# Kernel optimization log

Measured on AMD Instinct MI355X. Metric: run time of the kernel, lower is better.

## Reference

```python
import jax, jax.numpy as jnp
import numpy as np

D_MODEL = 768
D_HIDDEN = 2048
N_HEADS = 12
D_HEAD = 64
REG_COEFF = 1e-3
EPS = 1e-6
BATCH = 4
SEQ = 128


def setup_inputs() -> dict:
    key = jax.random.key(0)
    ks = jax.random.split(key, 4)
    # kaiming_uniform_ on (fan_in, fan_out)-shaped tensors: bound = sqrt(6 / fan_in_torch)
    # (values only need to be plausible; exact init dist is irrelevant for the kernel baseline)
    s_enc = 1.0 / np.sqrt(D_MODEL)
    s_dec = 1.0 / np.sqrt(D_HIDDEN)
    return {
        "x": jax.random.normal(ks[0], (BATCH, SEQ, D_MODEL), dtype=jnp.float32),
        "W_encQ": jax.random.normal(ks[1], (D_MODEL, D_HIDDEN), dtype=jnp.float32) * s_enc,
        "W_encK": jax.random.normal(ks[2], (D_MODEL, D_HIDDEN), dtype=jnp.float32) * s_enc,
        "b_encQ": jnp.zeros((D_HIDDEN,), dtype=jnp.float32),
        "b_encK": jnp.zeros((D_HIDDEN,), dtype=jnp.float32),
        "W_dec": jax.random.normal(ks[3], (D_HIDDEN, N_HEADS), dtype=jnp.float32) * s_dec,
        "b_dec": jnp.zeros((N_HEADS,), dtype=jnp.float32),
    }


def reference(x, W_encQ, W_encK, b_encQ, b_encK, W_dec, b_dec):
    # queries/keys: (batch, posn, d_hidden)
    queries = jax.nn.relu(jnp.einsum("bsd,dh->bsh", x, W_encQ) + b_encQ)
    keys = jax.nn.relu(jnp.einsum("bsd,dh->bsh", x, W_encK) + b_encK)
    # acts: (batch, posn_q, posn_k, d_hidden) -- the huge multi-use intermediate
    acts = queries[:, :, None, :] * keys[:, None, :, :]
    reg_loss = REG_COEFF * jnp.sum(jnp.sqrt(jnp.abs(acts) + EPS))
    feature_fires = (acts > 0).astype(jnp.int32)
    # decode to per-head scores: (batch, posn_q, posn_k, n_heads)
    score = jnp.einsum("bqkh,hn->bqkn", acts, W_dec) / np.sqrt(D_HEAD) + b_dec
    score = jnp.transpose(score, (0, 3, 1, 2))  # (batch, n_heads, posn_q, posn_k)
    return score, reg_loss, feature_fires
```

## Files before the change

### kernel.cpp

```cpp
#include <hip/hip_runtime.h>
#include <hip/hip_bf16.h>

#define D_MODEL 768
#define D_HIDDEN 2048
#define NHEADS 12
#define BATCH 4
#define SEQ 128
#define MROWS (BATCH*SEQ)
#define SCORE_ELEMS (BATCH*NHEADS*SEQ*SEQ)
#define REG_OFF SCORE_ELEMS
#define FIRES_OFF (SCORE_ELEMS + 1)
#define NROWS_T 65536
#define FIRES_WAVES 2048
#define FIRES_BLOCKS 512
#define SCORE_BLOCKS (BATCH*NHEADS*16)
#define REG_BLOCKS 512
#define TRIGCAP 64

typedef __attribute__((ext_vector_type(8))) short bf16x8;
typedef __attribute__((ext_vector_type(4))) float f32x4;

static __device__ __forceinline__ unsigned short f2bf(float f) {
    union { float f; unsigned u; } v; v.f = f;
    unsigned u = v.u;
    return (unsigned short)((u + 0x7FFFu + ((u >> 16) & 1u)) >> 16);
}

static __device__ __forceinline__ void split_bf16(float v, short& hi, short& lo) {
    unsigned short h = f2bf(v);
    float hf = __uint_as_float((unsigned)h << 16);
    float lf = v - hf;
    hi = (short)h;
    lo = (short)f2bf(lf);
}

static __device__ __forceinline__ float fsqrt_fast(float x) {
    return __builtin_amdgcn_sqrtf(x);
}

__global__ __launch_bounds__(256) void enc_kernel(
    const float* __restrict__ x,
    const float* __restrict__ WQ, const float* __restrict__ WK,
    const float* __restrict__ bQ, const float* __restrict__ bK,
    float* __restrict__ qbuf, float* __restrict__ kbuf,
    float* __restrict__ out)
{
    __shared__ unsigned tcnt;
    __shared__ unsigned tlist[TRIGCAP];
    __shared__ double   redd[4];

    const int bufid = blockIdx.z;
    const float* W    = bufid ? WK : WQ;
    const float* bias = bufid ? bK : bQ;
    float* outbuf     = bufid ? kbuf : qbuf;

    const int t  = threadIdx.x;
    if (t == 0) tcnt = 0u;
    if (blockIdx.x == 0 && blockIdx.y == 0 && blockIdx.z == 0 && t == 0)
        out[REG_OFF] = 0.f;
    __syncthreads();

    const int w  = t >> 6;
    const int l  = t & 63;
    const int mt = blockIdx.y * 64 + (w >> 1) * 32;
    const int nt = blockIdx.x * 64 + (w & 1) * 32;
    const int lr = l & 15;
    const int hg = (l >> 4) * 8;

    f32x4 acc[2][2];
    #pragma unroll
    for (int i = 0; i < 2; ++i)
        #pragma unroll
        for (int j = 0; j < 2; ++j) { f32x4 z = {0.f, 0.f, 0.f, 0.f}; acc[i][j] = z; }

    for (int kk = 0; kk < D_MODEL; kk += 32) {
        const int h0 = kk + hg;
        bf16x8 ah[2], al[2], bh[2], bl[2];
        #pragma unroll
        for (int fi = 0; fi < 2; ++fi) {
            const float* xp = x + (size_t)(mt + fi * 16 + lr) * D_MODEL + h0;
            const float4 v1 = *reinterpret_cast<const float4*>(xp);
            const float4 v2 = *reinterpret_cast<const float4*>(xp + 4);
            const float vv[8] = {v1.x, v1.y, v1.z, v1.w, v2.x, v2.y, v2.z, v2.w};
            #pragma unroll
            for (int i = 0; i < 8; ++i) {
                short h_, lo_;
                split_bf16(vv[i], h_, lo_);
                ah[fi][i] = h_; al[fi][i] = lo_;
            }
        }
        #pragma unroll
        for (int fj = 0; fj < 2; ++fj) {
            const int col = nt + fj * 16 + lr;
            #pragma unroll
            for (int i = 0; i < 8; ++i) {
                short h_, lo_;
                split_bf16(W[(size_t)(h0 + i) * D_HIDDEN + col], h_, lo_);
                bh[fj][i] = h_; bl[fj][i] = lo_;
            }
        }
        #pragma unroll
        for (int fi = 0; fi < 2; ++fi)
            #pragma unroll
            for (int fj = 0; fj < 2; ++fj) {
                acc[fi][fj] = __builtin_amdgcn_mfma_f32_16x16x32_bf16(
                    ah[fi], bh[fj], acc[fi][fj], 0, 0, 0);
                acc[fi][fj] = __builtin_amdgcn_mfma_f32_16x16x32_bf16(
                    ah[fi], bl[fj], acc[fi][fj], 0, 0, 0);
                acc[fi][fj] = __builtin_amdgcn_mfma_f32_16x16x32_bf16(
                    al[fi], bh[fj], acc[fi][fj], 0, 0, 0);
            }
    }

    #pragma unroll
    for (int fi = 0; fi < 2; ++fi)
        #pragma unroll
        for (int fj = 0; fj < 2; ++fj)
            #pragma unroll
            for (int j = 0; j < 4; ++j) {
                const int row = mt + fi * 16 + (l >> 4) * 4 + j;
                const int col = nt + fj * 16 + lr;
                float pre = acc[fi][fj][j] + bias[col];
                if (fabsf(pre) < 3e-4f) {
                    unsigned idx = atomicAdd(&tcnt, 1u);
                    if (idx < TRIGCAP) {
                        tlist[idx] = ((unsigned)row << 11) | (unsigned)col;
                    } else {
                        const float* xr = x + (size_t)row * D_MODEL;
                        const float* wc = W + col;
                        double s = (double)bias[col];
                        for (int dd = 0; dd < D_MODEL; ++dd)
                            s += (double)xr[dd] * (double)wc[(size_t)dd * D_HIDDEN];
                        pre = (float)s;
                    }
                }
                outbuf[(size_t)row * D_HIDDEN + col] = fmaxf(pre, 0.f);
            }

    __syncthreads();
    const unsigned n = min(tcnt, (unsigned)TRIGCAP);
    for (unsigned i = 0; i < n; ++i) {
        const unsigned e = tlist[i];
        const int hh = (int)(e & 2047u);
        const int mm = (int)(e >> 11);
        double s = 0.0;
        #pragma unroll
        for (int k = 0; k < 3; ++k) {
            const int dd = t + k * 256;
            s += (double)x[(size_t)mm * D_MODEL + dd]
               * (double)W[(size_t)dd * D_HIDDEN + hh];
        }
        #pragma unroll
        for (int off = 32; off > 0; off >>= 1) s += __shfl_down(s, off);
        if (l == 0) redd[w] = s;
        __syncthreads();
        if (t == 0) {
            double tot = redd[0] + redd[1] + redd[2] + redd[3] + (double)bias[hh];
            outbuf[(size_t)mm * D_HIDDEN + hh] = fmaxf((float)tot, 0.f);
        }
        __syncthreads();
    }
}

__global__ __launch_bounds__(128) void mask_kernel(
    const float* __restrict__ qbuf, const float* __restrict__ kbuf,
    unsigned* __restrict__ qmask, unsigned* __restrict__ kmask)
{
    const int r = blockIdx.x;
    const int t = threadIdx.x;
    const int l = t & 63;
    const float* src = (t < 64) ? qbuf : kbuf;
    unsigned* dst    = (t < 64) ? qmask : kmask;
    unsigned m = 0;
    #pragma unroll
    for (int j = 0; j < 8; ++j)
        #pragma unroll
        for (int e = 0; e < 4; ++e) {
            const float v = src[(size_t)r * D_HIDDEN + 256 * j + 4 * l + e];
            m |= (v > 0.f ? 1u : 0u) << (4 * j + e);
        }
    dst[r * 64 + l] = m;
}

__global__ __launch_bounds__(256) void main_kernel(
    const float* __restrict__ qbuf, const float* __restrict__ kbuf,
    const unsigned* __restrict__ qmask, const unsigned* __restrict__ kmask,
    const float* __restrict__ Wdec, const float* __restrict__ bdec,
    float* __restrict__ out)
{
    __shared__ float wcol[D_HIDDEN];
    __shared__ float red[4][64][16];
    __shared__ float rs[4];
    const int t  = threadIdx.x;
    const int bi = blockIdx.x;
    const int w  = t >> 6;
    const int l  = t & 63;

    if (bi < FIRES_BLOCKS) {
        const int g  = bi * 4 + w;
        const int g7 = g >> 7;
        const int gk = g & 127;

        f32x4* out4 = reinterpret_cast<f32x4*>(out + FIRES_OFF - 1);

        #pragma unroll 1
        for (int b = 0; b < 4; ++b) {
            const unsigned km = kmask[(b * SEQ + gk) * 64 + l];

            #pragma unroll 1
            for (int ss = 0; ss < 8; ++ss) {
                const int s    = b * 8 + ss;
                const int R    = g + s * FIRES_WAVES;
                const int brow = s * 16 + g7;
                const unsigned qm = qmask[brow * 64 + l];
                const unsigned m   = qm & km;
                const unsigned mp  = __shfl_up(m, 1);
                const unsigned m63 = __shfl(m, 63);

                unsigned pb1 = 0;
                if (l == 0 && R > 0) {
                    const int pbrow = (R - 1) >> 7;
                    const int pb    = pbrow >> 7;
                    const int pkrow = (pb << 7) + ((R - 1) & 127);
                    pb1 = (qmask[pbrow * 64 + 63] >> 31)
                        & (kmask[pkrow * 64 + 63] >> 31) & 1u;
                }

                #pragma unroll
                for (int j = 0; j < 8; ++j) {
                    unsigned b0;
                    if (l == 0) b0 = (j == 0) ? pb1 : (m63 >> (4 * (j - 1) + 3)) & 1u;
                    else        b0 = (mp >> (4 * j + 3)) & 1u;
                    f32x4 f;
                    f[0] = b0 ? 1.f : 0.f;
                    f[1] = ((m >> (4 * j + 0)) & 1u) ? 1.f : 0.f;
                    f[2] = ((m >> (4 * j + 1)) & 1u) ? 1.f : 0.f;
                    f[3] = ((m >> (4 * j + 2)) & 1u) ? 1.f : 0.f;
                    if (R == 0 && j == 0 && l == 0) {
                        out[FIRES_OFF + 0] = f[1];
                        out[FIRES_OFF + 1] = f[2];
                        out[FIRES_OFF + 2] = f[3];
                    } else {
                        out4[(size_t)R * 512 + 64 * j + l] = f;
                    }
                }
            }
        }

        if (bi == FIRES_BLOCKS - 1 && w == 3 && l == 0) {
            const float pv = qbuf[(size_t)511 * D_HIDDEN + 2047]
                           * kbuf[(size_t)511 * D_HIDDEN + 2047];
            out[(size_t)(FIRES_OFF - 1) + (size_t)NROWS_T * D_HIDDEN] = (pv > 0.f) ? 1.f : 0.f;
        }
        return;
    }

    if (bi < FIRES_BLOCKS + SCORE_BLOCKS) {
        const int sb  = bi - FIRES_BLOCKS;
        const int sub = sb & 15;
        const int pr  = sb >> 4;
        const int n   = pr % NHEADS;
        const int b   = pr / NHEADS;

        for (int idx = t; idx < D_HIDDEN; idx += 256)
            wcol[idx] = Wdec[(size_t)idx * NHEADS + n];
        __syncthreads();

        const int qt   = (sub >> 2) * 32;
        const int kt   = (sub & 3) * 32;
        const int lrow = l & 15;
        const int koff = (l >> 4) * 8;

        f32x4 acc[2][2];
        #pragma unroll
        for (int i = 0; i < 2; ++i)
            #pragma unroll
            for (int j = 0; j < 2; ++j) { f32x4 z = {0.f, 0.f, 0.f, 0.f}; acc[i][j] = z; }

        const float* qb = qbuf + (size_t)b * SEQ * D_HIDDEN;
        const float* kb = kbuf + (size_t)b * SEQ * D_HIDDEN;

        const int hlo = w * 512;
        for (int kk = hlo; kk < hlo + 512; kk += 32) {
            const int h0 = kk + koff;
            float wv[8];
            #pragma unroll
            for (int i = 0; i < 8; ++i) wv[i] = wcol[h0 + i];

            bf16x8 afrag[2], bfrag[2];
            #pragma unroll
            for (int fi = 0; fi < 2; ++fi) {
                const float* qp = qb + (size_t)(qt + fi * 16 + lrow) * D_HIDDEN + h0;
                const float4 q1 = *reinterpret_cast<const float4*>(qp);
                const float4 q2 = *reinterpret_cast<const float4*>(qp + 4);
                const float qf[8] = {q1.x, q1.y, q1.z, q1.w, q2.x, q2.y, q2.z, q2.w};
                #pragma unroll
                for (int i = 0; i < 8; ++i) afrag[fi][i] = (short)f2bf(qf[i] * wv[i]);
            }
            #pragma unroll
            for (int fj = 0; fj < 2; ++fj) {
                const float* kp = kb + (size_t)(kt + fj * 16 + lrow) * D_HIDDEN + h0;
                const float4 k1 = *reinterpret_cast<const float4*>(kp);
                const float4 k2 = *reinterpret_cast<const float4*>(kp + 4);
                const float kf[8] = {k1.x, k1.y, k1.z, k1.w, k2.x, k2.y, k2.z, k2.w};
                #pragma unroll
                for (int i = 0; i < 8; ++i) bfrag[fj][i] = (short)f2bf(kf[i]);
            }
            #pragma unroll
            for (int fi = 0; fi < 2; ++fi)
                #pragma unroll
                for (int fj = 0; fj < 2; ++fj)
                    acc[fi][fj] = __builtin_amdgcn_mfma_f32_16x16x32_bf16(
                        afrag[fi], bfrag[fj], acc[fi][fj], 0, 0, 0);
        }

        #pragma unroll
        for (int fi = 0; fi < 2; ++fi)
            #pragma unroll
            for (int fj = 0; fj < 2; ++fj)
                #pragma unroll
                for (int j = 0; j < 4; ++j)
                    red[w][l][fi * 8 + fj * 4 + j] = acc[fi][fj][j];
        __syncthreads();

        const float bd   = bdec[n];
        const int   outb = (b * NHEADS + n) * SEQ * SEQ;
        #pragma unroll
        for (int u = 0; u < 4; ++u) {
            const int j = w * 4 + u;
            const float s = (red[0][l][j] + red[1][l][j])
                          + (red[2][l][j] + red[3][l][j]);
            const int fi = j >> 3, fj = (j >> 2) & 1, jj = j & 3;
            const int row = qt + fi * 16 + (l >> 4) * 4 + jj;
            const int col = kt + fj * 16 + (l & 15);
            out[outb + row * SEQ + col] = s * 0.125f + bd;
        }
        return;
    }

    {
        const int qr = bi - FIRES_BLOCKS - SCORE_BLOCKS;
        const int b  = qr >> 7;
        const float* qrow = qbuf + (size_t)qr * D_HIDDEN + t * 8;
        const f32x4 q1 = *reinterpret_cast<const f32x4*>(qrow);
        const f32x4 q2 = *reinterpret_cast<const f32x4*>(qrow + 4);

        float acc = 0.f;
        #pragma unroll 1
        for (int k = 0; k < SEQ; ++k) {
            const float* kp = kbuf + (size_t)(b * SEQ + k) * D_HIDDEN + t * 8;
            const f32x4 k1 = *reinterpret_cast<const f32x4*>(kp);
            const f32x4 k2 = *reinterpret_cast<const f32x4*>(kp + 4);
            float s = 0.f;
            #pragma unroll
            for (int e = 0; e < 4; ++e) s += fsqrt_fast(q1[e] * k1[e] + 1e-6f);
            #pragma unroll
            for (int e = 0; e < 4; ++e) s += fsqrt_fast(q2[e] * k2[e] + 1e-6f);
            acc += s;
        }

        #pragma unroll
        for (int off = 32; off > 0; off >>= 1) acc += __shfl_down(acc, off);
        if (l == 0) rs[w] = acc;
        __syncthreads();
        if (t == 0)
            atomicAdd(out + REG_OFF, ((rs[0] + rs[1]) + (rs[2] + rs[3])) * 1e-3f);
    }
}

extern "C" void kernel_launch(void* const* d_in, const int* in_sizes, int n_in,
                              void* d_out, int out_size, void* d_ws, size_t ws_size,
                              hipStream_t stream) {
    const float* x  = (const float*)d_in[0];
    const float* WQ = (const float*)d_in[1];
    const float* WK = (const float*)d_in[2];
    const float* bQ = (const float*)d_in[3];
    const float* bK = (const float*)d_in[4];
    const float* Wd = (const float*)d_in[5];
    const float* bd = (const float*)d_in[6];
    float* out  = (float*)d_out;
    float* qbuf = (float*)d_ws;
    float* kbuf = qbuf + (size_t)MROWS * D_HIDDEN;
    unsigned* qmask = (unsigned*)(kbuf + (size_t)MROWS * D_HIDDEN);
    unsigned* kmask = qmask + (size_t)MROWS * 64;

    dim3 b256(256);

    enc_kernel<<<dim3(D_HIDDEN / 64, MROWS / 64, 2), b256, 0, stream>>>(
        x, WQ, WK, bQ, bK, qbuf, kbuf, out);

    mask_kernel<<<dim3(MROWS), dim3(128), 0, stream>>>(qbuf, kbuf, qmask, kmask);

    main_kernel<<<dim3(FIRES_BLOCKS + SCORE_BLOCKS + REG_BLOCKS), b256, 0, stream>>>(
        qbuf, kbuf, qmask, kmask, Wd, bd, out);
}
```

Measured before the change: 196.8 us.

## Factor reg loss into per-feature sqrt sums and nonzero counts

The reg-loss path no longer evaluates sqrt(q*k+eps) over every (q,k,h) triple. It uses the factorisation sqrt(q*k) = sqrt(q)*sqrt(k), summing sqrt values and nonzero counts per batch and feature in a prep kernel, and treats each zero product as contributing sqrt(eps). A single block then combines these sums in double precision. Fires stores are also switched to nontemporal writes. The trade-off is an extra memset and atomics, plus an approximation where the eps term is dropped for nonzero products.

```diff
diff --git a/kernel.cpp b/kernel.cpp
--- a/kernel.cpp
+++ b/kernel.cpp
@@ -14,7 +14,6 @@
 #define FIRES_WAVES 2048
 #define FIRES_BLOCKS 512
 #define SCORE_BLOCKS (BATCH*NHEADS*16)
-#define REG_BLOCKS 512
 #define TRIGCAP 64
 
 typedef __attribute__((ext_vector_type(8))) short bf16x8;
@@ -42,8 +41,7 @@
     const float* __restrict__ x,
     const float* __restrict__ WQ, const float* __restrict__ WK,
     const float* __restrict__ bQ, const float* __restrict__ bK,
-    float* __restrict__ qbuf, float* __restrict__ kbuf,
-    float* __restrict__ out)
+    float* __restrict__ qbuf, float* __restrict__ kbuf)
 {
     __shared__ unsigned tcnt;
     __shared__ unsigned tlist[TRIGCAP];
@@ -56,8 +54,6 @@
 
     const int t  = threadIdx.x;
     if (t == 0) tcnt = 0u;
-    if (blockIdx.x == 0 && blockIdx.y == 0 && blockIdx.z == 0 && t == 0)
-        out[REG_OFF] = 0.f;
     __syncthreads();
 
     const int w  = t >> 6;
@@ -162,35 +158,76 @@
     }
 }
 
-__global__ __launch_bounds__(128) void mask_kernel(
+__global__ __launch_bounds__(256) void prep_kernel(
     const float* __restrict__ qbuf, const float* __restrict__ kbuf,
-    unsigned* __restrict__ qmask, unsigned* __restrict__ kmask)
+    unsigned* __restrict__ qmask, unsigned* __restrict__ kmask,
+    float* __restrict__ sq, float* __restrict__ sk,
+    float* __restrict__ nzq, float* __restrict__ nzk)
 {
-    const int r = blockIdx.x;
-    const int t = threadIdx.x;
-    const int l = t & 63;
-    const float* src = (t < 64) ? qbuf : kbuf;
-    unsigned* dst    = (t < 64) ? qmask : kmask;
-    unsigned m = 0;
+    const int bi = blockIdx.x;
+    const int t  = threadIdx.x;
+
+    if (bi < MROWS) {
+        if (t >= 128) return;
+        const int r = bi;
+        const int l = t & 63;
+        const float* src = (t < 64) ? qbuf : kbuf;
+        unsigned* dst    = (t < 64) ? qmask : kmask;
+        unsigned m = 0;
+        #pragma unroll
+        for (int j = 0; j < 8; ++j)
+            #pragma unroll
+            for (int e = 0; e < 4; ++e) {
+                const float v = src[(size_t)r * D_HIDDEN + 256 * j + 4 * l + e];
+                m |= (v > 0.f ? 1u : 0u) << (4 * j + e);
+            }
+        dst[r * 64 + l] = m;
+        return;
+    }
+
+    const int cid = bi - MROWS;
+    const int buf = cid >> 6;
+    const int idx = cid & 63;
+    const int b   = idx >> 4;
+    const int rg  = idx & 15;
+    const float* src = buf ? kbuf : qbuf;
+    float* S  = buf ? sk  : sq;
+    float* NZ = buf ? nzk : nzq;
+
+    const int h0 = t * 8;
+    float s[8]  = {0, 0, 0, 0, 0, 0, 0, 0};
+    float nz[8] = {0, 0, 0, 0, 0, 0, 0, 0};
     #pragma unroll
-    for (int j = 0; j < 8; ++j)
+    for (int rr = 0; rr < 8; ++rr) {
+        const int row = b * SEQ + rg * 8 + rr;
+        const float* p = src + (size_t)row * D_HIDDEN + h0;
+        const f32x4 v1 = *reinterpret_cast<const f32x4*>(p);
+        const f32x4 v2 = *reinterpret_cast<const f32x4*>(p + 4);
         #pragma unroll
         for (int e = 0; e < 4; ++e) {
-            const float v = src[(size_t)r * D_HIDDEN + 256 * j + 4 * l + e];
-            m |= (v > 0.f ? 1u : 0u) << (4 * j + e);
-        }
-    dst[r * 64 + l] = m;
+            s[e]      += fsqrt_fast(v1[e]);
+            nz[e]     += (v1[e] > 0.f) ? 1.f : 0.f;
+            s[e + 4]  += fsqrt_fast(v2[e]);
+            nz[e + 4] += (v2[e] > 0.f) ? 1.f : 0.f;
+        }
+    }
+    #pragma unroll
+    for (int e = 0; e < 8; ++e) {
+        atomicAdd(&S[b * D_HIDDEN + h0 + e], s[e]);
+        atomicAdd(&NZ[b * D_HIDDEN + h0 + e], nz[e]);
+    }
 }
 
 __global__ __launch_bounds__(256) void main_kernel(
     const float* __restrict__ qbuf, const float* __restrict__ kbuf,
     const unsigned* __restrict__ qmask, const unsigned* __restrict__ kmask,
+    const float* __restrict__ sq, const float* __restrict__ sk,
+    const float* __restrict__ nzq, const float* __restrict__ nzk,
     const float* __restrict__ Wdec, const float* __restrict__ bdec,
     float* __restrict__ out)
 {
     __shared__ float wcol[D_HIDDEN];
     __shared__ float red[4][64][16];
-    __shared__ float rs[4];
     const int t  = threadIdx.x;
     const int bi = blockIdx.x;
     const int w  = t >> 6;
@@ -241,7 +278,7 @@
                         out[FIRES_OFF + 1] = f[2];
                         out[FIRES_OFF + 2] = f[3];
                     } else {
-                        out4[(size_t)R * 512 + 64 * j + l] = f;
+                        __builtin_nontemporal_store(f, &out4[(size_t)R * 512 + 64 * j + l]);
                     }
                 }
             }
@@ -339,32 +376,18 @@
     }
 
     {
-        const int qr = bi - FIRES_BLOCKS - SCORE_BLOCKS;
-        const int b  = qr >> 7;
-        const float* qrow = qbuf + (size_t)qr * D_HIDDEN + t * 8;
-        const f32x4 q1 = *reinterpret_cast<const f32x4*>(qrow);
-        const f32x4 q2 = *reinterpret_cast<const f32x4*>(qrow + 4);
-
-        float acc = 0.f;
-        #pragma unroll 1
-        for (int k = 0; k < SEQ; ++k) {
-            const float* kp = kbuf + (size_t)(b * SEQ + k) * D_HIDDEN + t * 8;
-            const f32x4 k1 = *reinterpret_cast<const f32x4*>(kp);
-            const f32x4 k2 = *reinterpret_cast<const f32x4*>(kp + 4);
-            float s = 0.f;
-            #pragma unroll
-            for (int e = 0; e < 4; ++e) s += fsqrt_fast(q1[e] * k1[e] + 1e-6f);
-            #pragma unroll
-            for (int e = 0; e < 4; ++e) s += fsqrt_fast(q2[e] * k2[e] + 1e-6f);
-            acc += s;
-        }
-
+        __shared__ double rd[4];
+        double acc = 0.0;
+        for (int i = t; i < BATCH * D_HIDDEN; i += 256) {
+            const float zc = 16384.f - nzq[i] * nzk[i];
+            acc += (double)(sq[i] * sk[i] + zc * 1e-3f);
+        }
         #pragma unroll
         for (int off = 32; off > 0; off >>= 1) acc += __shfl_down(acc, off);
-        if (l == 0) rs[w] = acc;
+        if (l == 0) rd[w] = acc;
         __syncthreads();
         if (t == 0)
-            atomicAdd(out + REG_OFF, ((rs[0] + rs[1]) + (rs[2] + rs[3])) * 1e-3f);
+            out[REG_OFF] = (float)((rd[0] + rd[1] + rd[2] + rd[3]) * 1e-3);
     }
 }
 
@@ -383,14 +406,21 @@
     float* kbuf = qbuf + (size_t)MROWS * D_HIDDEN;
     unsigned* qmask = (unsigned*)(kbuf + (size_t)MROWS * D_HIDDEN);
     unsigned* kmask = qmask + (size_t)MROWS * 64;
+    float* sq  = (float*)(kmask + (size_t)MROWS * 64);
+    float* sk  = sq  + BATCH * D_HIDDEN;
+    float* nzq = sk  + BATCH * D_HIDDEN;
+    float* nzk = nzq + BATCH * D_HIDDEN;
 
     dim3 b256(256);
 
+    (void)hipMemsetAsync(sq, 0, (size_t)4 * BATCH * D_HIDDEN * sizeof(float), stream);
+
     enc_kernel<<<dim3(D_HIDDEN / 64, MROWS / 64, 2), b256, 0, stream>>>(
-        x, WQ, WK, bQ, bK, qbuf, kbuf, out);
-
-    mask_kernel<<<dim3(MROWS), dim3(128), 0, stream>>>(qbuf, kbuf, qmask, kmask);
-
-    main_kernel<<<dim3(FIRES_BLOCKS + SCORE_BLOCKS + REG_BLOCKS), b256, 0, stream>>>(
-        qbuf, kbuf, qmask, kmask, Wd, bd, out);
-}
+        x, WQ, WK, bQ, bK, qbuf, kbuf);
+
+    prep_kernel<<<dim3(MROWS + 128), b256, 0, stream>>>(
+        qbuf, kbuf, qmask, kmask, sq, sk, nzq, nzk);
+
+    main_kernel<<<dim3(FIRES_BLOCKS + SCORE_BLOCKS + 1), b256, 0, stream>>>(
+        qbuf, kbuf, qmask, kmask, sq, sk, nzq, nzk, Wd, bd, out);
+}
```

Measured after the change: 171.3 us. 1.15x faster.
